# Kernel optimization log

Measured on AMD Instinct MI355X. Metric: run time of the kernel, lower is better.

The kernel has to match this reference:

```python
import jax, jax.numpy as jnp
from jax import lax
import numpy as np


def _gru_cell(x, h, wih, whh, bih, bhh):
    # torch.nn.GRUCell math: gates split order (r, z, n)
    gi = x @ wih.T + bih          # (N, 3H)
    gh = h @ whh.T + bhh          # (N, 3H)
    ir, iz, i_n = jnp.split(gi, 3, axis=-1)
    hr, hz, h_n = jnp.split(gh, 3, axis=-1)
    r = jax.nn.sigmoid(ir + hr)
    z = jax.nn.sigmoid(iz + hz)
    n = jnp.tanh(i_n + r * h_n)
    return (1.0 - z) * n + z * h


def _dilated_gru(x, dilation, wih, whh, bih, bhh):
    # h_i depends on h_{i-dilation} -> `dilation` independent chains,
    # scanned jointly with a carried state of shape (B*dilation, H).
    B, S, I = x.shape
    H = whh.shape[1]
    nc = S // dilation  # assumes S % dilation == 0
    xr = x.reshape(B, nc, dilation, I).transpose(1, 0, 2, 3).reshape(nc, B * dilation, I)

    def step(h, xt):
        hn = _gru_cell(xt, h, wih, whh, bih, bhh)
        return hn, hn

    h0 = jnp.zeros((B * dilation, H), x.dtype)
    _, ys = lax.scan(step, h0, xr)  # (nc, B*dilation, H)
    return ys.reshape(nc, B, dilation, H).transpose(1, 0, 2, 3).reshape(B, S, H)


def _encoder(data, fparams, bparams, dilations):
    outs = []
    x = data
    for p, d in zip(fparams, dilations):
        x = _dilated_gru(x, d, *p)
        outs.append(x[:, -1, :])
    x = data[:, ::-1, :]
    for p, d in zip(bparams, dilations):
        x = _dilated_gru(x, d, *p)
        outs.append(x[:, -1, :])
    return jnp.concatenate(outs, axis=1)  # (B, 2*sum(hidden_sizes)) = (B, 400)


def setup_inputs() -> dict:
    key = jax.random.key(0)
    ks = jax.random.split(key, 7)
    B, S = 1024, 512
    sizes = [(1, 100), (100, 50), (50, 50)]  # (input_size, hidden_size) per layer

    def cell(k, iS, H):
        k1, k2, k3, k4 = jax.random.split(k, 4)
        s = 1.0 / np.sqrt(H)  # torch GRUCell init: U(-1/sqrt(H), 1/sqrt(H))
        u = lambda kk, shp: jax.random.uniform(kk, shp, jnp.float32, -s, s)
        return u(k1, (3 * H, iS)), u(k2, (3 * H, H)), u(k3, (3 * H,)), u(k4, (3 * H,))

    d = {"data": jax.random.normal(ks[0], (B, S, 1), jnp.float32)}
    for i, nm in enumerate(["f1", "f2", "f3", "b1", "b2", "b3"]):
        iS, H = sizes[i % 3]
        w1, w2, bb1, bb2 = cell(ks[i + 1], iS, H)
        d[nm + "_wih"] = w1
        d[nm + "_whh"] = w2
        d[nm + "_bih"] = bb1
        d[nm + "_bhh"] = bb2
    return d


def reference(data,
              f1_wih, f1_whh, f1_bih, f1_bhh,
              f2_wih, f2_whh, f2_bih, f2_bhh,
              f3_wih, f3_whh, f3_bih, f3_bhh,
              b1_wih, b1_whh, b1_bih, b1_bhh,
              b2_wih, b2_whh, b2_bih, b2_bhh,
              b3_wih, b3_whh, b3_bih, b3_bhh):
    dilations = (1, 4, 16)
    fparams = [(f1_wih, f1_whh, f1_bih, f1_bhh),
               (f2_wih, f2_whh, f2_bih, f2_bhh),
               (f3_wih, f3_whh, f3_bih, f3_bhh)]
    bparams = [(b1_wih, b1_whh, b1_bih, b1_bhh),
               (b2_wih, b2_whh, b2_bih, b2_bhh),
               (b3_wih, b3_whh, b3_bih, b3_bhh)]
    return _encoder(data, fparams, bparams, dilations)
```

## Files before the change

### kernel.cpp

```cpp
#include <hip/hip_runtime.h>
#include <math.h>

typedef short  s16x8 __attribute__((ext_vector_type(8)));
typedef float  f32x4 __attribute__((ext_vector_type(4)));

static __device__ __forceinline__ float sigf(float x){ return 1.0f/(1.0f+__expf(-x)); }
static __device__ __forceinline__ float tanhf_fast(float x){
  float ax=fabsf(x); float e=__expf(-2.0f*ax); float t=(1.0f-e)/(1.0f+e); return copysignf(t,x);
}
static __device__ __forceinline__ unsigned short f2bf(float x){
  unsigned int u = __float_as_uint(x);
  unsigned int r = (u + 0x7FFFu + ((u >> 16) & 1u)) >> 16;
  return (unsigned short)r;
}
static __device__ __forceinline__ float bf2f(unsigned short b){
  return __uint_as_float(((unsigned int)b) << 16);
}
static __device__ __forceinline__ unsigned int cvt_pk_bf16(float a, float b){
  unsigned int r;
  asm("v_cvt_pk_bf16_f32 %0, %1, %2" : "=v"(r) : "v"(a), "v"(b));
  return r;
}
static __device__ __forceinline__ void fast_barrier(){
  asm volatile("s_waitcnt lgkmcnt(0)" ::: "memory");
// ... 6 lines not shown
}
static __device__ __forceinline__ float rsum4(float v){
  return v + __int_as_float(__builtin_amdgcn_ds_swizzle(__float_as_int(v), 0x101F));
}
static __device__ __forceinline__ float sel4(int c, float4 v){
  float r=v.x; r=(c==1)?v.y:r; r=(c==2)?v.z:r; r=(c==3)?v.w:r; return r;
}

static __device__ __forceinline__ void load_afrag(const float* __restrict__ whh,
                                                  int gate, int tile, int l, int kc,
                                                  s16x8& hi, s16x8& lo){
  const int r  = tile*16 + (l & 15);
  const int kb = kc*32 + (l >> 4)*8;
  #pragma unroll
  for (int j = 0; j < 8; ++j){
    const int k = kb + j;
    const float wv = (r < 100 && k < 100) ? whh[(size_t)(gate*100 + r)*100 + k] : 0.0f;
    const unsigned short hb = f2bf(wv);
    hi[j] = (short)hb;
    lo[j] = (short)f2bf(wv - bf2f(hb));
  }
}

__global__ __launch_bounds__(448, 2)
void gru_l1(const float* __restrict__ data,
            const float* __restrict__ wih_f, const float* __restrict__ whh_f,
            const float* __restrict__ bih_f, const float* __restrict__ bhh_f,
            const float* __restrict__ wih_b, const float* __restrict__ whh_b,
            const float* __restrict__ bih_b, const float* __restrict__ bhh_b,
            float* __restrict__ x1f, float* __restrict__ x1b,
            float* __restrict__ out)
{
  const int dir   = (int)(blockIdx.x >> 6);
  const int blk16 = (int)(blockIdx.x & 63);
  const int t     = (int)threadIdx.x;
  const float* __restrict__ wih = dir ? wih_b : wih_f;
  const float* __restrict__ whh = dir ? whh_b : whh_f;
  const float* __restrict__ bih = dir ? bih_b : bih_f;
  const float* __restrict__ bhh = dir ? bhh_b : bhh_f;
  float* __restrict__ x1 = dir ? x1b : x1f;
  const int obase = dir ? 200 : 0;
  const int b0 = blk16 * 16;

  __shared__ __align__(16) unsigned short hBhi[2][16][136];
  __shared__ __align__(16) unsigned short hBlo[2][16][136];
  __shared__ __align__(16) float xs[512][16];

  for (int i = t; i < 8192; i += 448){
    const int c  = i >> 9;
    const int sL = i & 511;
    xs[sL][c] = data[(size_t)(b0 + c)*512 + (size_t)(dir ? (511 - sL) : sL)];
  }
  { unsigned short* ph = (unsigned short*)hBhi;
    unsigned short* pl = (unsigned short*)hBlo;
    for (int i = t; i < 2*16*136; i += 448){ ph[i] = 0; pl[i] = 0; } }

  const int l  = t & 63;
  const int W  = t >> 6;

  s16x8 AH00,AH01,AH02,AH03, AH10,AH11,AH12,AH13, AH20,AH21,AH22,AH23;
  s16x8 AL00,AL01,AL02,AL03, AL10,AL11,AL12,AL13, AL20,AL21,AL22,AL23;
  #define LDA(G,KC) load_afrag(whh, G, W, l, KC, AH##G##KC, AL##G##KC);
  LDA(0,0) LDA(0,1) LDA(0,2) LDA(0,3)
  LDA(1,0) LDA(1,1) LDA(1,2) LDA(1,3)
  LDA(2,0) LDA(2,1) LDA(2,2) LDA(2,3)
  #undef LDA

  const int mg  = (l >> 4) * 4;
  const int u0  = W*16 + mg;
  const bool uvalid = (u0 < 100);
  const int u0c = uvalid ? u0 : 96;
  const int c   = l & 15;
  const f32x4 wxr4 = *(const f32x4*)&wih[u0c];
  const f32x4 wxz4 = *(const f32x4*)&wih[100 + u0c];
  const f32x4 wxn4 = *(const f32x4*)&wih[200 + u0c];
  const f32x4 bcr4 = *(const f32x4*)&bih[u0c]       + *(const f32x4*)&bhh[u0c];
  const f32x4 bcz4 = *(const f32x4*)&bih[100 + u0c] + *(const f32x4*)&bhh[100 + u0c];
  const f32x4 bxn4 = *(const f32x4*)&bih[200 + u0c];
  const f32x4 bhn4 = *(const f32x4*)&bhh[200 + u0c];
  f32x4 hprev = {0.f,0.f,0.f,0.f};

  __syncthreads();

  const int bn = c;
  const int bg = (l >> 4)*8;

  #pragma unroll 1
  for (int s = 0; s < 512; ++s){
    const int cur = s & 1, nxt = cur ^ 1;

    const s16x8 BH0 = *(const s16x8*)&hBhi[cur][bn][ 0 + bg];
    const s16x8 BL0 = *(const s16x8*)&hBlo[cur][bn][ 0 + bg];
    const s16x8 BH1 = *(const s16x8*)&hBhi[cur][bn][32 + bg];
    const s16x8 BL1 = *(const s16x8*)&hBlo[cur][bn][32 + bg];
    const s16x8 BH2 = *(const s16x8*)&hBhi[cur][bn][64 + bg];
    const s16x8 BL2 = *(const s16x8*)&hBlo[cur][bn][64 + bg];
    const s16x8 BH3 = *(const s16x8*)&hBhi[cur][bn][96 + bg];
    const s16x8 BL3 = *(const s16x8*)&hBlo[cur][bn][96 + bg];

    f32x4 Ca0={0.f,0.f,0.f,0.f}, Cb0={0.f,0.f,0.f,0.f};
    f32x4 Ca1={0.f,0.f,0.f,0.f}, Cb1={0.f,0.f,0.f,0.f};
    f32x4 Ca2={0.f,0.f,0.f,0.f}, Cb2={0.f,0.f,0.f,0.f};
    #define MM(ACC,G,KC) \
      ACC = __builtin_amdgcn_mfma_f32_16x16x32_bf16(AL##G##KC, BH##KC, ACC, 0, 0, 0); \
      ACC = __builtin_amdgcn_mfma_f32_16x16x32_bf16(AH##G##KC, BL##KC, ACC, 0, 0, 0); \
      ACC = __builtin_amdgcn_mfma_f32_16x16x32_bf16(AH##G##KC, BH##KC, ACC, 0, 0, 0);
    MM(Ca0,0,0) MM(Ca1,1,0) MM(Ca2,2,0)
    MM(Cb0,0,2) MM(Cb1,1,2) MM(Cb2,2,2)
    MM(Ca0,0,1) MM(Ca1,1,1) MM(Ca2,2,1)
    MM(Cb0,0,3) MM(Cb1,1,3) MM(Cb2,2,3)
    #undef MM
    const f32x4 sr = Ca0 + Cb0;
    const f32x4 sz = Ca1 + Cb1;
    const f32x4 sn = Ca2 + Cb2;

    const float xc = xs[s][c];
    f32x4 hn;
    #define FIN(I) { \
      const float rr = sigf(sr[I] + fmaf(wxr4[I], xc, bcr4[I])); \
      const float zz = sigf(sz[I] + fmaf(wxz4[I], xc, bcz4[I])); \
      const float nn = tanhf_fast(fmaf(wxn4[I], xc, bxn4[I]) + rr*(sn[I] + bhn4[I])); \
      hn[I] = nn + zz*(hprev[I] - nn); }
    FIN(0) FIN(1) FIN(2) FIN(3)
    #undef FIN
    hprev = hn;

    if (uvalid){
      const unsigned int px = cvt_pk_bf16(hn[0], hn[1]);
      const unsigned int py = cvt_pk_bf16(hn[2], hn[3]);
      const float l0 = hn[0] - __uint_as_float(px << 16);
      const float l1 = hn[1] - __uint_as_float(px & 0xFFFF0000u);
      const float l2 = hn[2] - __uint_as_float(py << 16);
      const float l3 = hn[3] - __uint_as_float(py & 0xFFFF0000u);
      uint2 vhi; vhi.x = px; vhi.y = py;
      uint2 vlo; vlo.x = cvt_pk_bf16(l0, l1); vlo.y = cvt_pk_bf16(l2, l3);
      *(uint2*)&hBhi[nxt][c][u0] = vhi;
      *(uint2*)&hBlo[nxt][c][u0] = vlo;
      if ((s & 3) == 3){
        const int cs = s >> 2;
        const int ch = b0 + c;
        const size_t base = (((size_t)cs*256 + (ch >> 2))*100);
        x1[(base + u0 + 0)*4 + (ch & 3)] = hn[0];
        x1[(base + u0 + 1)*4 + (ch & 3)] = hn[1];
        x1[(base + u0 + 2)*4 + (ch & 3)] = hn[2];
        x1[(base + u0 + 3)*4 + (ch & 3)] = hn[3];
      }
      if (s == 511){
        const int ch = b0 + c;
        *(f32x4*)&out[(size_t)ch*400 + obase + u0] = hn;
      }
    }
    fast_barrier();
  }
}

static __device__ __forceinline__ float l2w(const float* __restrict__ wih,
                                            const float* __restrict__ whh,
                                            int sec, int r, int k){
  if (r >= 50) return 0.f;
  if (sec == 2) return (k < 100) ? wih[(size_t)(100 + r)*100 + k] : 0.f;
  if (sec == 3) return (k >= 104 && k < 154) ? whh[(size_t)(100 + r)*50 + (k - 104)] : 0.f;
  const int ro = (sec == 1) ? 50 : 0;
  if (k < 100) return wih[(size_t)(ro + r)*100 + k];
  if (k >= 104 && k < 154) return whh[(size_t)(ro + r)*50 + (k - 104)];
  return 0.f;
}
static __device__ __forceinline__ void l2_afrag(const float* __restrict__ wih,
                                                const float* __restrict__ whh,
                                                int sec, int tile, int l, int kc,
                                                s16x8& hi, s16x8& lo){
  const int r  = tile*16 + (l & 15);
  const int kb = kc*32 + (l >> 4)*8;
  #pragma unroll
  for (int j = 0; j < 8; ++j){
    const float wv = l2w(wih, whh, sec, r, kb + j);
    const unsigned short hb = f2bf(wv);
    hi[j] = (short)hb;
    lo[j] = (short)f2bf(wv - bf2f(hb));
  }
}

__global__ __launch_bounds__(256, 1)
void gru_l2(const float* __restrict__ x1f, const float* __restrict__ x1b,
            const float* __restrict__ wih_f, const float* __restrict__ whh_f,
            const float* __restrict__ bih_f, const float* __restrict__ bhh_f,
            const float* __restrict__ wih_b, const float* __restrict__ whh_b,
            const float* __restrict__ bih_b, const float* __restrict__ bhh_b,
            float* __restrict__ x2f, float* __restrict__ x2b,
            float* __restrict__ out)
{
  const int dir   = (int)(blockIdx.x >> 6);
  const int blk16 = (int)(blockIdx.x & 63);
  const int t     = (int)threadIdx.x;
  const float* __restrict__ wih = dir ? wih_b : wih_f;
  const float* __restrict__ whh = dir ? whh_b : whh_f;
  const float* __restrict__ bih = dir ? bih_b : bih_f;
  const float* __restrict__ bhh = dir ? bhh_b : bhh_f;
  const float* __restrict__ x1 = dir ? x1b : x1f;
  float* __restrict__ x2 = dir ? x2b : x2f;
  const int obase = dir ? 300 : 100;
  const int b0 = blk16 * 16;

  __shared__ __align__(16) unsigned short hBhi[2][16][168];
  __shared__ __align__(16) unsigned short hBlo[2][16][168];

  { unsigned short* ph = (unsigned short*)hBhi;
    unsigned short* pl = (unsigned short*)hBlo;
    for (int i = t; i < 2*16*168; i += 256){ ph[i] = 0; pl[i] = 0; } }

  const int l = t & 63;
  const int W = t >> 6;

  s16x8 AH00,AH01,AH02,AH03,AH04, AH10,AH11,AH12,AH13,AH14,
        AH20,AH21,AH22,AH23,AH24, AH30,AH31,AH32,AH33,AH34;
  s16x8 AL00,AL01,AL02,AL03,AL04, AL10,AL11,AL12,AL13,AL14,
        AL20,AL21,AL22,AL23,AL24, AL30,AL31,AL32,AL33,AL34;
  #define LDA(SE,KC) l2_afrag(wih, whh, SE, W, l, KC, AH##SE##KC, AL##SE##KC);
  LDA(0,0) LDA(0,1) LDA(0,2) LDA(0,3) LDA(0,4)
  LDA(1,0) LDA(1,1) LDA(1,2) LDA(1,3) LDA(1,4)
  LDA(2,0) LDA(2,1) LDA(2,2) LDA(2,3) LDA(2,4)
  LDA(3,0) LDA(3,1) LDA(3,2) LDA(3,3) LDA(3,4)
  #undef LDA

  const int mg = (l >> 4) * 4;
  const int c  = l & 15;
  const int u0 = W*16 + mg;
  const int ch = b0 + c;
  f32x4 bcr, bcz, bxn, bhn;
  #pragma unroll
  for (int i = 0; i < 4; ++i){
    const int u = (u0 + i < 50) ? (u0 + i) : 49;
    bcr[i] = bih[u]      + bhh[u];
    bcz[i] = bih[50 + u] + bhh[50 + u];
    bxn[i] = bih[100 + u];
    bhn[i] = bhh[100 + u];
  }
  const bool vH = (u0 < 50);
  f32x4 hp = {0.f,0.f,0.f,0.f};

  float* px = x2 + (((size_t)(ch >> 2))*50 + u0)*4 + (ch & 3);
  const size_t X2STRIDE = (size_t)256*50*4;

  const int oct  = t >> 4;
  const int cc   = t & 15;
  const bool stg = (t < 208);
  const int u0x  = oct * 8;

  __syncthreads();

  if (stg){
    const float* p = x1 + ((size_t)0*256 + (b0 >> 2) + (cc >> 2))*400 + (cc & 3);
    float xv[8];
    #pragma unroll
    for (int j = 0; j < 8; ++j){
      const int uu = u0x + j;
      xv[j] = (uu < 100) ? p[4*uu] : 0.f;
    }
    unsigned int h0 = cvt_pk_bf16(xv[0], xv[1]);
    unsigned int h1 = cvt_pk_bf16(xv[2], xv[3]);
    unsigned int h2 = cvt_pk_bf16(xv[4], xv[5]);
    unsigned int h3 = cvt_pk_bf16(xv[6], xv[7]);
    uint4 vhi; vhi.x=h0; vhi.y=h1; vhi.z=h2; vhi.w=h3;
    uint4 vlo;
    vlo.x = cvt_pk_bf16(xv[0]-__uint_as_float(h0<<16), xv[1]-__uint_as_float(h0&0xFFFF0000u));
    vlo.y = cvt_pk_bf16(xv[2]-__uint_as_float(h1<<16), xv[3]-__uint_as_float(h1&0xFFFF0000u));
    vlo.z = cvt_pk_bf16(xv[4]-__uint_as_float(h2<<16), xv[5]-__uint_as_float(h2&0xFFFF0000u));
    vlo.w = cvt_pk_bf16(xv[6]-__uint_as_float(h3<<16), xv[7]-__uint_as_float(h3&0xFFFF0000u));
    *(uint4*)&hBhi[0][cc][u0x] = vhi;
    *(uint4*)&hBlo[0][cc][u0x] = vlo;
  }
  __syncthreads();

  const int bn = c;
  const int bg = (l >> 4)*8;

  #pragma unroll 1
  for (int s = 0; s < 128; ++s){
    const int cur = s & 1, nxt = cur ^ 1;

    float xv0=0,xv1=0,xv2=0,xv3=0,xv4=0,xv5=0,xv6=0,xv7=0;
    if (stg){
      const int st = (s + 1 < 128) ? (s + 1) : 127;
      const float* p = x1 + ((size_t)st*256 + (b0 >> 2) + (cc >> 2))*400 + (cc & 3);
      #define XL(J, V) { const int uu = u0x + (J); \
        V = (uu < 100) ? p[4*uu] : 0.f; }
      XL(0,xv0) XL(1,xv1) XL(2,xv2) XL(3,xv3) XL(4,xv4) XL(5,xv5) XL(6,xv6) XL(7,xv7)
      #undef XL
    }

    const s16x8 BH0 = *(const s16x8*)&hBhi[cur][bn][  0 + bg];
    const s16x8 BL0 = *(const s16x8*)&hBlo[cur][bn][  0 + bg];
    const s16x8 BH1 = *(const s16x8*)&hBhi[cur][bn][ 32 + bg];
    const s16x8 BL1 = *(const s16x8*)&hBlo[cur][bn][ 32 + bg];
    const s16x8 BH2 = *(const s16x8*)&hBhi[cur][bn][ 64 + bg];
    const s16x8 BL2 = *(const s16x8*)&hBlo[cur][bn][ 64 + bg];
    const s16x8 BH3 = *(const s16x8*)&hBhi[cur][bn][ 96 + bg];
    const s16x8 BL3 = *(const s16x8*)&hBlo[cur][bn][ 96 + bg];
    const s16x8 BH4 = *(const s16x8*)&hBhi[cur][bn][128 + bg];
    const s16x8 BL4 = *(const s16x8*)&hBlo[cur][bn][128 + bg];

    f32x4 CrA={0.f,0.f,0.f,0.f}, CzA={0.f,0.f,0.f,0.f}, CxA={0.f,0.f,0.f,0.f}, ChA={0.f,0.f,0.f,0.f};
    f32x4 CrB={0.f,0.f,0.f,0.f}, CzB={0.f,0.f,0.f,0.f}, CxB={0.f,0.f,0.f,0.f}, ChB={0.f,0.f,0.f,0.f};
    #define MF(ACC,A,B) ACC = __builtin_amdgcn_mfma_f32_16x16x32_bf16(A, B, ACC, 0, 0, 0);
    #define G4(SET,KC,AOP,BOP) \
      MF(Cr##SET, AOP##0##KC, BOP##KC) MF(Cz##SET, AOP##1##KC, BOP##KC) \
      MF(Cx##SET, AOP##2##KC, BOP##KC) MF(Ch##SET, AOP##3##KC, BOP##KC)
    G4(A,0,AL,BH) G4(B,3,AL,BH) G4(A,1,AL,BH) G4(B,4,AL,BH) G4(A,2,AL,BH)
    G4(A,0,AH,BL) G4(B,3,AH,BL) G4(A,1,AH,BL) G4(B,4,AH,BL) G4(A,2,AH,BL)
    G4(A,0,AH,BH) G4(B,3,AH,BH) G4(A,1,AH,BH) G4(B,4,AH,BH) G4(A,2,AH,BH)
    #undef G4
    #undef MF
    const f32x4 Cr = CrA + CrB;
    const f32x4 Cz = CzA + CzB;
    const f32x4 Cx = CxA + CxB;
    const f32x4 Ch = ChA + ChB;

    f32x4 hn;
    #define FIN(I) { \
      const float rr = sigf(Cr[I] + bcr[I]); \
      const float zz = sigf(Cz[I] + bcz[I]); \
      const float nn = tanhf_fast(Cx[I] + bxn[I] + rr*(Ch[I] + bhn[I])); \
      hn[I] = nn + zz*(hp[I] - nn); }
    FIN(0) FIN(1) FIN(2) FIN(3)
    #undef FIN
    hp = hn;

    if (vH){
      const unsigned int p0 = cvt_pk_bf16(hn[0], hn[1]);
      const unsigned int p1 = cvt_pk_bf16(hn[2], hn[3]);
      const float l0 = hn[0] - __uint_as_float(p0 << 16);
      const float l1 = hn[1] - __uint_as_float(p0 & 0xFFFF0000u);
      const float l2 = hn[2] - __uint_as_float(p1 << 16);
      const float l3 = hn[3] - __uint_as_float(p1 & 0xFFFF0000u);
      uint2 whi; whi.x = p0; whi.y = p1;
      uint2 wlo; wlo.x = cvt_pk_bf16(l0, l1); wlo.y = cvt_pk_bf16(l2, l3);
      *(uint2*)&hBhi[nxt][c][104 + u0] = whi;
      *(uint2*)&hBlo[nxt][c][104 + u0] = wlo;
      if ((s & 3) == 3){
        if (u0 + 0 < 50) px[ 0] = hn[0];
        if (u0 + 1 < 50) px[ 4] = hn[1];
        if (u0 + 2 < 50) px[ 8] = hn[2];
        if (u0 + 3 < 50) px[12] = hn[3];
        px += X2STRIDE;
      }
      if (s == 127){
        if (u0 + 0 < 50) out[(size_t)ch*400 + obase + u0 + 0] = hn[0];
        if (u0 + 1 < 50) out[(size_t)ch*400 + obase + u0 + 1] = hn[1];
        if (u0 + 2 < 50) out[(size_t)ch*400 + obase + u0 + 2] = hn[2];
        if (u0 + 3 < 50) out[(size_t)ch*400 + obase + u0 + 3] = hn[3];
      }
    }

    if (stg){
      unsigned int h0 = cvt_pk_bf16(xv0, xv1);
      unsigned int h1 = cvt_pk_bf16(xv2, xv3);
      unsigned int h2 = cvt_pk_bf16(xv4, xv5);
      unsigned int h3 = cvt_pk_bf16(xv6, xv7);
      uint4 vhi; vhi.x=h0; vhi.y=h1; vhi.z=h2; vhi.w=h3;
      uint4 vlo;
      vlo.x = cvt_pk_bf16(xv0-__uint_as_float(h0<<16), xv1-__uint_as_float(h0&0xFFFF0000u));
      vlo.y = cvt_pk_bf16(xv2-__uint_as_float(h1<<16), xv3-__uint_as_float(h1&0xFFFF0000u));
      vlo.z = cvt_pk_bf16(xv4-__uint_as_float(h2<<16), xv5-__uint_as_float(h2&0xFFFF0000u));
      vlo.w = cvt_pk_bf16(xv6-__uint_as_float(h3<<16), xv7-__uint_as_float(h3&0xFFFF0000u));
      *(uint4*)&hBhi[nxt][cc][u0x] = vhi;
      *(uint4*)&hBlo[nxt][cc][u0x] = vlo;
    }
    fast_barrier();
  }
}

__global__ __launch_bounds__(512, 4)
void gru_l3(const float* __restrict__ x2f, const float* __restrict__ x2b,
            const float* __restrict__ wih_f, const float* __restrict__ whh_f,
            const float* __restrict__ bih_f, const float* __restrict__ bhh_f,
            const float* __restrict__ wih_b, const float* __restrict__ whh_b,
            const float* __restrict__ bih_b, const float* __restrict__ bhh_b,
            float* __restrict__ out)
{
  const int dir = (int)(blockIdx.x >> 8);
  const int blk = (int)(blockIdx.x & 255);
  const int t   = (int)threadIdx.x;
  const float* __restrict__ wih = dir ? wih_b : wih_f;
  const float* __restrict__ whh = dir ? whh_b : whh_f;
  const float* __restrict__ bih = dir ? bih_b : bih_f;
  const float* __restrict__ bhh = dir ? bhh_b : bhh_f;
  const float* __restrict__ x2 = dir ? x2b : x2f;
  const int obase = dir ? 350 : 150;
  const int b0 = blk * 4;

  __shared__ __align__(16) float xh[2][104][4];
// ... 85 lines not shown
  const float* f2_whh = (const float*)d_in[6];
  const float* f2_bih = (const float*)d_in[7];
  const float* f2_bhh = (const float*)d_in[8];
  const float* f3_wih = (const float*)d_in[9];
  const float* f3_whh = (const float*)d_in[10];
  const float* f3_bih = (const float*)d_in[11];
  const float* f3_bhh = (const float*)d_in[12];
  const float* b1_wih = (const float*)d_in[13];
  const float* b1_whh = (const float*)d_in[14];
  const float* b1_bih = (const float*)d_in[15];
  const float* b1_bhh = (const float*)d_in[16];
  const float* b2_wih = (const float*)d_in[17];
  const float* b2_whh = (const float*)d_in[18];
  const float* b2_bih = (const float*)d_in[19];
  const float* b2_bhh = (const float*)d_in[20];
  const float* b3_wih = (const float*)d_in[21];
  const float* b3_whh = (const float*)d_in[22];
  const float* b3_bih = (const float*)d_in[23];
  const float* b3_bhh = (const float*)d_in[24];
  float* out = (float*)d_out;

  const size_t X1N = (size_t)128 * 256 * 100 * 4;
  const size_t X2N = (size_t)32 * 256 * 50 * 4;
  if (ws_size < (2 * X1N + 2 * X2N) * sizeof(float)) return;
  float* wsf = (float*)d_ws;
  float* x1f = wsf;
  float* x1b = wsf + X1N;
  float* x2f = wsf + 2 * X1N;
  float* x2b = wsf + 2 * X1N + X2N;

  gru_l1<<<dim3(128), dim3(448), 0, stream>>>(
      data, f1_wih, f1_whh, f1_bih, f1_bhh,
      b1_wih, b1_whh, b1_bih, b1_bhh, x1f, x1b, out);
  gru_l2<<<dim3(128), dim3(256), 0, stream>>>(
      x1f, x1b, f2_wih, f2_whh, f2_bih, f2_bhh,
      b2_wih, b2_whh, b2_bih, b2_bhh, x2f, x2b, out);
  gru_l3<<<dim3(512), dim3(512), 0, stream>>>(
      x2f, x2b, f3_wih, f3_whh, f3_bih, f3_bhh,
      b3_wih, b3_whh, b3_bih, b3_bhh, out);
}
```

Measured before the change: 1.024 ms.

## Fuse layer-1 and layer-2 GRU kernels with flag-based producer-consumer pipelining

Merges the layer-1 and layer-2 kernels into one launch of 256 blocks. The first 128 blocks run layer 1 and publish per-block progress flags with release stores every 4 steps. The other 128 blocks run layer 2 and spin on those flags with acquire loads before reading each x1 chunk. This lets layer 2 overlap with layer 1 instead of waiting for it to finish, removing most of the layer-2 serial time. The cost is extra barriers and a vmcnt wait in layer 1, spin-wait overhead, and reliance on all 256 blocks being co-resident to avoid deadlock, with a spin budget as a fallback.

```diff
diff --git a/kernel.cpp b/kernel.cpp
--- a/kernel.cpp
+++ b/kernel.cpp
@@ -52,138 +52,6 @@
   }
 }
 
-__global__ __launch_bounds__(448, 2)
-void gru_l1(const float* __restrict__ data,
-            const float* __restrict__ wih_f, const float* __restrict__ whh_f,
-            const float* __restrict__ bih_f, const float* __restrict__ bhh_f,
-            const float* __restrict__ wih_b, const float* __restrict__ whh_b,
-            const float* __restrict__ bih_b, const float* __restrict__ bhh_b,
-            float* __restrict__ x1f, float* __restrict__ x1b,
-            float* __restrict__ out)
-{
-  const int dir   = (int)(blockIdx.x >> 6);
-  const int blk16 = (int)(blockIdx.x & 63);
-  const int t     = (int)threadIdx.x;
-  const float* __restrict__ wih = dir ? wih_b : wih_f;
-  const float* __restrict__ whh = dir ? whh_b : whh_f;
-  const float* __restrict__ bih = dir ? bih_b : bih_f;
-  const float* __restrict__ bhh = dir ? bhh_b : bhh_f;
-  float* __restrict__ x1 = dir ? x1b : x1f;
-  const int obase = dir ? 200 : 0;
-  const int b0 = blk16 * 16;
-
-  __shared__ __align__(16) unsigned short hBhi[2][16][136];
-  __shared__ __align__(16) unsigned short hBlo[2][16][136];
-  __shared__ __align__(16) float xs[512][16];
-
-  for (int i = t; i < 8192; i += 448){
-    const int c  = i >> 9;
-    const int sL = i & 511;
-    xs[sL][c] = data[(size_t)(b0 + c)*512 + (size_t)(dir ? (511 - sL) : sL)];
-  }
-  { unsigned short* ph = (unsigned short*)hBhi;
-    unsigned short* pl = (unsigned short*)hBlo;
-    for (int i = t; i < 2*16*136; i += 448){ ph[i] = 0; pl[i] = 0; } }
-
-  const int l  = t & 63;
-  const int W  = t >> 6;
-
-  s16x8 AH00,AH01,AH02,AH03, AH10,AH11,AH12,AH13, AH20,AH21,AH22,AH23;
-  s16x8 AL00,AL01,AL02,AL03, AL10,AL11,AL12,AL13, AL20,AL21,AL22,AL23;
-  #define LDA(G,KC) load_afrag(whh, G, W, l, KC, AH##G##KC, AL##G##KC);
-  LDA(0,0) LDA(0,1) LDA(0,2) LDA(0,3)
-  LDA(1,0) LDA(1,1) LDA(1,2) LDA(1,3)
-  LDA(2,0) LDA(2,1) LDA(2,2) LDA(2,3)
-  #undef LDA
-
-  const int mg  = (l >> 4) * 4;
-  const int u0  = W*16 + mg;
-  const bool uvalid = (u0 < 100);
-  const int u0c = uvalid ? u0 : 96;
-  const int c   = l & 15;
-  const f32x4 wxr4 = *(const f32x4*)&wih[u0c];
-  const f32x4 wxz4 = *(const f32x4*)&wih[100 + u0c];
-  const f32x4 wxn4 = *(const f32x4*)&wih[200 + u0c];
-  const f32x4 bcr4 = *(const f32x4*)&bih[u0c]       + *(const f32x4*)&bhh[u0c];
-  const f32x4 bcz4 = *(const f32x4*)&bih[100 + u0c] + *(const f32x4*)&bhh[100 + u0c];
-  const f32x4 bxn4 = *(const f32x4*)&bih[200 + u0c];
-  const f32x4 bhn4 = *(const f32x4*)&bhh[200 + u0c];
-  f32x4 hprev = {0.f,0.f,0.f,0.f};
-
-  __syncthreads();
-
-  const int bn = c;
-  const int bg = (l >> 4)*8;
-
-  #pragma unroll 1
-  for (int s = 0; s < 512; ++s){
-    const int cur = s & 1, nxt = cur ^ 1;
-
-    const s16x8 BH0 = *(const s16x8*)&hBhi[cur][bn][ 0 + bg];
-    const s16x8 BL0 = *(const s16x8*)&hBlo[cur][bn][ 0 + bg];
-    const s16x8 BH1 = *(const s16x8*)&hBhi[cur][bn][32 + bg];
-    const s16x8 BL1 = *(const s16x8*)&hBlo[cur][bn][32 + bg];
-    const s16x8 BH2 = *(const s16x8*)&hBhi[cur][bn][64 + bg];
-    const s16x8 BL2 = *(const s16x8*)&hBlo[cur][bn][64 + bg];
-    const s16x8 BH3 = *(const s16x8*)&hBhi[cur][bn][96 + bg];
-    const s16x8 BL3 = *(const s16x8*)&hBlo[cur][bn][96 + bg];
-
-    f32x4 Ca0={0.f,0.f,0.f,0.f}, Cb0={0.f,0.f,0.f,0.f};
-    f32x4 Ca1={0.f,0.f,0.f,0.f}, Cb1={0.f,0.f,0.f,0.f};
-    f32x4 Ca2={0.f,0.f,0.f,0.f}, Cb2={0.f,0.f,0.f,0.f};
-    #define MM(ACC,G,KC) \
-      ACC = __builtin_amdgcn_mfma_f32_16x16x32_bf16(AL##G##KC, BH##KC, ACC, 0, 0, 0); \
-      ACC = __builtin_amdgcn_mfma_f32_16x16x32_bf16(AH##G##KC, BL##KC, ACC, 0, 0, 0); \
-      ACC = __builtin_amdgcn_mfma_f32_16x16x32_bf16(AH##G##KC, BH##KC, ACC, 0, 0, 0);
-    MM(Ca0,0,0) MM(Ca1,1,0) MM(Ca2,2,0)
-    MM(Cb0,0,2) MM(Cb1,1,2) MM(Cb2,2,2)
-    MM(Ca0,0,1) MM(Ca1,1,1) MM(Ca2,2,1)
-    MM(Cb0,0,3) MM(Cb1,1,3) MM(Cb2,2,3)
-    #undef MM
-    const f32x4 sr = Ca0 + Cb0;
-    const f32x4 sz = Ca1 + Cb1;
-    const f32x4 sn = Ca2 + Cb2;
-
-    const float xc = xs[s][c];
-    f32x4 hn;
-    #define FIN(I) { \
-      const float rr = sigf(sr[I] + fmaf(wxr4[I], xc, bcr4[I])); \
-      const float zz = sigf(sz[I] + fmaf(wxz4[I], xc, bcz4[I])); \
-      const float nn = tanhf_fast(fmaf(wxn4[I], xc, bxn4[I]) + rr*(sn[I] + bhn4[I])); \
-      hn[I] = nn + zz*(hprev[I] - nn); }
-    FIN(0) FIN(1) FIN(2) FIN(3)
-    #undef FIN
-    hprev = hn;
-
-    if (uvalid){
-      const unsigned int px = cvt_pk_bf16(hn[0], hn[1]);
-      const unsigned int py = cvt_pk_bf16(hn[2], hn[3]);
-      const float l0 = hn[0] - __uint_as_float(px << 16);
-      const float l1 = hn[1] - __uint_as_float(px & 0xFFFF0000u);
-      const float l2 = hn[2] - __uint_as_float(py << 16);
-      const float l3 = hn[3] - __uint_as_float(py & 0xFFFF0000u);
-      uint2 vhi; vhi.x = px; vhi.y = py;
-      uint2 vlo; vlo.x = cvt_pk_bf16(l0, l1); vlo.y = cvt_pk_bf16(l2, l3);
-      *(uint2*)&hBhi[nxt][c][u0] = vhi;
-      *(uint2*)&hBlo[nxt][c][u0] = vlo;
-      if ((s & 3) == 3){
-        const int cs = s >> 2;
-        const int ch = b0 + c;
-        const size_t base = (((size_t)cs*256 + (ch >> 2))*100);
-        x1[(base + u0 + 0)*4 + (ch & 3)] = hn[0];
-        x1[(base + u0 + 1)*4 + (ch & 3)] = hn[1];
-        x1[(base + u0 + 2)*4 + (ch & 3)] = hn[2];
-        x1[(base + u0 + 3)*4 + (ch & 3)] = hn[3];
-      }
-      if (s == 511){
-        const int ch = b0 + c;
-        *(f32x4*)&out[(size_t)ch*400 + obase + u0] = hn;
-      }
-    }
-    fast_barrier();
-  }
-}
-
 static __device__ __forceinline__ float l2w(const float* __restrict__ wih,
                                             const float* __restrict__ whh,
                                             int sec, int r, int k){
@@ -210,192 +78,346 @@
   }
 }
 
-__global__ __launch_bounds__(256, 1)
-void gru_l2(const float* __restrict__ x1f, const float* __restrict__ x1b,
-            const float* __restrict__ wih_f, const float* __restrict__ whh_f,
-            const float* __restrict__ bih_f, const float* __restrict__ bhh_f,
-            const float* __restrict__ wih_b, const float* __restrict__ whh_b,
-            const float* __restrict__ bih_b, const float* __restrict__ bhh_b,
-            float* __restrict__ x2f, float* __restrict__ x2b,
-            float* __restrict__ out)
+__global__ __launch_bounds__(448, 2)
+void gru_fused(const float* __restrict__ data,
+               const float* __restrict__ w1ih_f, const float* __restrict__ w1hh_f,
+               const float* __restrict__ b1ih_f, const float* __restrict__ b1hh_f,
+               const float* __restrict__ w1ih_b, const float* __restrict__ w1hh_b,
+               const float* __restrict__ b1ih_b, const float* __restrict__ b1hh_b,
+               const float* __restrict__ w2ih_f, const float* __restrict__ w2hh_f,
+               const float* __restrict__ b2ih_f, const float* __restrict__ b2hh_f,
+               const float* __restrict__ w2ih_b, const float* __restrict__ w2hh_b,
+               const float* __restrict__ b2ih_b, const float* __restrict__ b2hh_b,
+               float* __restrict__ x1f, float* __restrict__ x1b,
+               float* __restrict__ x2f, float* __restrict__ x2b,
+               int* __restrict__ flags,
+               float* __restrict__ out)
 {
-  const int dir   = (int)(blockIdx.x >> 6);
-  const int blk16 = (int)(blockIdx.x & 63);
-  const int t     = (int)threadIdx.x;
-  const float* __restrict__ wih = dir ? wih_b : wih_f;
-  const float* __restrict__ whh = dir ? whh_b : whh_f;
-  const float* __restrict__ bih = dir ? bih_b : bih_f;
-  const float* __restrict__ bhh = dir ? bhh_b : bhh_f;
-  const float* __restrict__ x1 = dir ? x1b : x1f;
-  float* __restrict__ x2 = dir ? x2b : x2f;
-  const int obase = dir ? 300 : 100;
-  const int b0 = blk16 * 16;
-
-  __shared__ __align__(16) unsigned short hBhi[2][16][168];
-  __shared__ __align__(16) unsigned short hBlo[2][16][168];
-
-  { unsigned short* ph = (unsigned short*)hBhi;
-    unsigned short* pl = (unsigned short*)hBlo;
-    for (int i = t; i < 2*16*168; i += 256){ ph[i] = 0; pl[i] = 0; } }
-
-  const int l = t & 63;
-  const int W = t >> 6;
-
-  s16x8 AH00,AH01,AH02,AH03,AH04, AH10,AH11,AH12,AH13,AH14,
-        AH20,AH21,AH22,AH23,AH24, AH30,AH31,AH32,AH33,AH34;
-  s16x8 AL00,AL01,AL02,AL03,AL04, AL10,AL11,AL12,AL13,AL14,
-        AL20,AL21,AL22,AL23,AL24, AL30,AL31,AL32,AL33,AL34;
-  #define LDA(SE,KC) l2_afrag(wih, whh, SE, W, l, KC, AH##SE##KC, AL##SE##KC);
-  LDA(0,0) LDA(0,1) LDA(0,2) LDA(0,3) LDA(0,4)
-  LDA(1,0) LDA(1,1) LDA(1,2) LDA(1,3) LDA(1,4)
-  LDA(2,0) LDA(2,1) LDA(2,2) LDA(2,3) LDA(2,4)
-  LDA(3,0) LDA(3,1) LDA(3,2) LDA(3,3) LDA(3,4)
-  #undef LDA
-
-  const int mg = (l >> 4) * 4;
-  const int c  = l & 15;
-  const int u0 = W*16 + mg;
-  const int ch = b0 + c;
-  f32x4 bcr, bcz, bxn, bhn;
-  #pragma unroll
-  for (int i = 0; i < 4; ++i){
-    const int u = (u0 + i < 50) ? (u0 + i) : 49;
-    bcr[i] = bih[u]      + bhh[u];
-    bcz[i] = bih[50 + u] + bhh[50 + u];
-    bxn[i] = bih[100 + u];
-    bhn[i] = bhh[100 + u];
-  }
-  const bool vH = (u0 < 50);
-  f32x4 hp = {0.f,0.f,0.f,0.f};
-
-  float* px = x2 + (((size_t)(ch >> 2))*50 + u0)*4 + (ch & 3);
-  const size_t X2STRIDE = (size_t)256*50*4;
-
-  const int oct  = t >> 4;
-  const int cc   = t & 15;
-  const bool stg = (t < 208);
-  const int u0x  = oct * 8;
-
-  __syncthreads();
-
-  if (stg){
-    const float* p = x1 + ((size_t)0*256 + (b0 >> 2) + (cc >> 2))*400 + (cc & 3);
-    float xv[8];
+  __shared__ __align__(16) char smem[50176];
+  const int t = (int)threadIdx.x;
+
+  if (blockIdx.x < 128){
+    const int dir   = (int)(blockIdx.x >> 6);
+    const int blk16 = (int)(blockIdx.x & 63);
+    const int fid   = (int)blockIdx.x;
+    const float* __restrict__ wih = dir ? w1ih_b : w1ih_f;
+    const float* __restrict__ whh = dir ? w1hh_b : w1hh_f;
+    const float* __restrict__ bih = dir ? b1ih_b : b1ih_f;
+    const float* __restrict__ bhh = dir ? b1hh_b : b1hh_f;
+    float* __restrict__ x1 = dir ? x1b : x1f;
+    const int obase = dir ? 200 : 0;
+    const int b0 = blk16 * 16;
+
+    unsigned short (*hBhi)[16][136] = (unsigned short (*)[16][136])(smem);
+    unsigned short (*hBlo)[16][136] = (unsigned short (*)[16][136])(smem + 8704);
+    float (*xs)[16]                 = (float (*)[16])(smem + 17408);
+
+    for (int i = t; i < 8192; i += 448){
+      const int c  = i >> 9;
+      const int sL = i & 511;
+      xs[sL][c] = data[(size_t)(b0 + c)*512 + (size_t)(dir ? (511 - sL) : sL)];
+    }
+    { unsigned short* ph = (unsigned short*)smem;
+      for (int i = t; i < 2*2*16*136; i += 448) ph[i] = 0; }
+
+    const int l  = t & 63;
+    const int W  = t >> 6;
+
+    s16x8 AH00,AH01,AH02,AH03, AH10,AH11,AH12,AH13, AH20,AH21,AH22,AH23;
+    s16x8 AL00,AL01,AL02,AL03, AL10,AL11,AL12,AL13, AL20,AL21,AL22,AL23;
+    #define LDA(G,KC) load_afrag(whh, G, W, l, KC, AH##G##KC, AL##G##KC);
+    LDA(0,0) LDA(0,1) LDA(0,2) LDA(0,3)
+    LDA(1,0) LDA(1,1) LDA(1,2) LDA(1,3)
+    LDA(2,0) LDA(2,1) LDA(2,2) LDA(2,3)
+    #undef LDA
+
+    const int mg  = (l >> 4) * 4;
+    const int u0  = W*16 + mg;
+    const bool uvalid = (u0 < 100);
+    const int u0c = uvalid ? u0 : 96;
+    const int c   = l & 15;
+    const f32x4 wxr4 = *(const f32x4*)&wih[u0c];
+    const f32x4 wxz4 = *(const f32x4*)&wih[100 + u0c];
+    const f32x4 wxn4 = *(const f32x4*)&wih[200 + u0c];
+    const f32x4 bcr4 = *(const f32x4*)&bih[u0c]       + *(const f32x4*)&bhh[u0c];
+    const f32x4 bcz4 = *(const f32x4*)&bih[100 + u0c] + *(const f32x4*)&bhh[100 + u0c];
+    const f32x4 bxn4 = *(const f32x4*)&bih[200 + u0c];
+    const f32x4 bhn4 = *(const f32x4*)&bhh[200 + u0c];
+    f32x4 hprev = {0.f,0.f,0.f,0.f};
+
+    __syncthreads();
+
+    const int bn = c;
+    const int bg = (l >> 4)*8;
+
+    #pragma unroll 1
+    for (int s = 0; s < 512; ++s){
+      const int cur = s & 1, nxt = cur ^ 1;
+
+      const s16x8 BH0 = *(const s16x8*)&hBhi[cur][bn][ 0 + bg];
+      const s16x8 BL0 = *(const s16x8*)&hBlo[cur][bn][ 0 + bg];
+      const s16x8 BH1 = *(const s16x8*)&hBhi[cur][bn][32 + bg];
+      const s16x8 BL1 = *(const s16x8*)&hBlo[cur][bn][32 + bg];
+      const s16x8 BH2 = *(const s16x8*)&hBhi[cur][bn][64 + bg];
+      const s16x8 BL2 = *(const s16x8*)&hBlo[cur][bn][64 + bg];
+      const s16x8 BH3 = *(const s16x8*)&hBhi[cur][bn][96 + bg];
+      const s16x8 BL3 = *(const s16x8*)&hBlo[cur][bn][96 + bg];
+
+      f32x4 Ca0={0.f,0.f,0.f,0.f}, Cb0={0.f,0.f,0.f,0.f};
+      f32x4 Ca1={0.f,0.f,0.f,0.f}, Cb1={0.f,0.f,0.f,0.f};
+      f32x4 Ca2={0.f,0.f,0.f,0.f}, Cb2={0.f,0.f,0.f,0.f};
+      #define MM(ACC,G,KC) \
+        ACC = __builtin_amdgcn_mfma_f32_16x16x32_bf16(AL##G##KC, BH##KC, ACC, 0, 0, 0); \
+        ACC = __builtin_amdgcn_mfma_f32_16x16x32_bf16(AH##G##KC, BL##KC, ACC, 0, 0, 0); \
+        ACC = __builtin_amdgcn_mfma_f32_16x16x32_bf16(AH##G##KC, BH##KC, ACC, 0, 0, 0);
+      MM(Ca0,0,0) MM(Ca1,1,0) MM(Ca2,2,0)
+      MM(Cb0,0,2) MM(Cb1,1,2) MM(Cb2,2,2)
+      MM(Ca0,0,1) MM(Ca1,1,1) MM(Ca2,2,1)
+      MM(Cb0,0,3) MM(Cb1,1,3) MM(Cb2,2,3)
+      #undef MM
+      const f32x4 sr = Ca0 + Cb0;
+      const f32x4 sz = Ca1 + Cb1;
+      const f32x4 sn = Ca2 + Cb2;
+
+      const float xc = xs[s][c];
+      f32x4 hn;
+      #define FIN(I) { \
+        const float rr = sigf(sr[I] + fmaf(wxr4[I], xc, bcr4[I])); \
+        const float zz = sigf(sz[I] + fmaf(wxz4[I], xc, bcz4[I])); \
+        const float nn = tanhf_fast(fmaf(wxn4[I], xc, bxn4[I]) + rr*(sn[I] + bhn4[I])); \
+        hn[I] = nn + zz*(hprev[I] - nn); }
+      FIN(0) FIN(1) FIN(2) FIN(3)
+      #undef FIN
+      hprev = hn;
+
+      if (uvalid){
+        const unsigned int px = cvt_pk_bf16(hn[0], hn[1]);
+        const unsigned int py = cvt_pk_bf16(hn[2], hn[3]);
+        const float l0 = hn[0] - __uint_as_float(px << 16);
+        const float l1 = hn[1] - __uint_as_float(px & 0xFFFF0000u);
+        const float l2 = hn[2] - __uint_as_float(py << 16);
+        const float l3 = hn[3] - __uint_as_float(py & 0xFFFF0000u);
+        uint2 vhi; vhi.x = px; vhi.y = py;
+        uint2 vlo; vlo.x = cvt_pk_bf16(l0, l1); vlo.y = cvt_pk_bf16(l2, l3);
+        *(uint2*)&hBhi[nxt][c][u0] = vhi;
+        *(uint2*)&hBlo[nxt][c][u0] = vlo;
+        if ((s & 3) == 3){
+          const int cs = s >> 2;
+          const int ch = b0 + c;
+          const size_t base = (((size_t)cs*256 + (ch >> 2))*100);
+          x1[(base + u0 + 0)*4 + (ch & 3)] = hn[0];
+          x1[(base + u0 + 1)*4 + (ch & 3)] = hn[1];
+          x1[(base + u0 + 2)*4 + (ch & 3)] = hn[2];
+          x1[(base + u0 + 3)*4 + (ch & 3)] = hn[3];
+        }
+        if (s == 511){
+          const int ch = b0 + c;
+          *(f32x4*)&out[(size_t)ch*400 + obase + u0] = hn;
+        }
+      }
+      if ((s & 3) == 3){
+        asm volatile("s_waitcnt vmcnt(0)" ::: "memory");
+        __builtin_amdgcn_s_barrier();
+        if (t == 0){
+          __hip_atomic_store(&flags[fid], (s >> 2) + 1,
+                             __ATOMIC_RELEASE, __HIP_MEMORY_SCOPE_AGENT);
+        }
+      }
+      fast_barrier();
+    }
+  } else {
+    const int kb    = (int)blockIdx.x - 128;
+    const int dir   = kb >> 6;
+    const int blk16 = kb & 63;
+    const int fid   = kb;
+    const float* __restrict__ wih = dir ? w2ih_b : w2ih_f;
+    const float* __restrict__ whh = dir ? w2hh_b : w2hh_f;
+    const float* __restrict__ bih = dir ? b2ih_b : b2ih_f;
+    const float* __restrict__ bhh = dir ? b2hh_b : b2hh_f;
+    const float* __restrict__ x1 = dir ? x1b : x1f;
+    float* __restrict__ x2 = dir ? x2b : x2f;
+    const int obase = dir ? 300 : 100;
+    const int b0 = blk16 * 16;
+
+    unsigned short (*hBhi)[16][168] = (unsigned short (*)[16][168])(smem);
+    unsigned short (*hBlo)[16][168] = (unsigned short (*)[16][168])(smem + 10752);
+
+    { unsigned short* ph = (unsigned short*)smem;
+      for (int i = t; i < 2*2*16*168; i += 448) ph[i] = 0; }
+
+    const int l = t & 63;
+    const int W = t >> 6;
+
+    s16x8 AH00,AH01,AH02,AH03,AH04, AH10,AH11,AH12,AH13,AH14,
+          AH20,AH21,AH22,AH23,AH24, AH30,AH31,AH32,AH33,AH34;
+    s16x8 AL00,AL01,AL02,AL03,AL04, AL10,AL11,AL12,AL13,AL14,
+          AL20,AL21,AL22,AL23,AL24, AL30,AL31,AL32,AL33,AL34;
+    #define LDA(SE,KC) l2_afrag(wih, whh, SE, W, l, KC, AH##SE##KC, AL##SE##KC);
+    LDA(0,0) LDA(0,1) LDA(0,2) LDA(0,3) LDA(0,4)
+    LDA(1,0) LDA(1,1) LDA(1,2) LDA(1,3) LDA(1,4)
+    LDA(2,0) LDA(2,1) LDA(2,2) LDA(2,3) LDA(2,4)
+    LDA(3,0) LDA(3,1) LDA(3,2) LDA(3,3) LDA(3,4)
+    #undef LDA
+
+    const int mg = (l >> 4) * 4;
+    const int c  = l & 15;
+    const int u0 = W*16 + mg;
+    const int ch = b0 + c;
+    f32x4 bcr, bcz, bxn, bhn;
     #pragma unroll
-    for (int j = 0; j < 8; ++j){
-      const int uu = u0x + j;
-      xv[j] = (uu < 100) ? p[4*uu] : 0.f;
-    }
-    unsigned int h0 = cvt_pk_bf16(xv[0], xv[1]);
-    unsigned int h1 = cvt_pk_bf16(xv[2], xv[3]);
-    unsigned int h2 = cvt_pk_bf16(xv[4], xv[5]);
-    unsigned int h3 = cvt_pk_bf16(xv[6], xv[7]);
-    uint4 vhi; vhi.x=h0; vhi.y=h1; vhi.z=h2; vhi.w=h3;
-    uint4 vlo;
-    vlo.x = cvt_pk_bf16(xv[0]-__uint_as_float(h0<<16), xv[1]-__uint_as_float(h0&0xFFFF0000u));
-    vlo.y = cvt_pk_bf16(xv[2]-__uint_as_float(h1<<16), xv[3]-__uint_as_float(h1&0xFFFF0000u));
-    vlo.z = cvt_pk_bf16(xv[4]-__uint_as_float(h2<<16), xv[5]-__uint_as_float(h2&0xFFFF0000u));
-    vlo.w = cvt_pk_bf16(xv[6]-__uint_as_float(h3<<16), xv[7]-__uint_as_float(h3&0xFFFF0000u));
-    *(uint4*)&hBhi[0][cc][u0x] = vhi;
-    *(uint4*)&hBlo[0][cc][u0x] = vlo;
-  }
-  __syncthreads();
-
-  const int bn = c;
-  const int bg = (l >> 4)*8;
-
-  #pragma unroll 1
-  for (int s = 0; s < 128; ++s){
-    const int cur = s & 1, nxt = cur ^ 1;
-
-    float xv0=0,xv1=0,xv2=0,xv3=0,xv4=0,xv5=0,xv6=0,xv7=0;
+    for (int i = 0; i < 4; ++i){
+      const int u = (u0 + i < 50) ? (u0 + i) : 49;
+      bcr[i] = bih[u]      + bhh[u];
+      bcz[i] = bih[50 + u] + bhh[50 + u];
+      bxn[i] = bih[100 + u];
+      bhn[i] = bhh[100 + u];
+    }
+    const bool vH = (u0 < 50);
+    f32x4 hp = {0.f,0.f,0.f,0.f};
+
+    float* px = x2 + (((size_t)(ch >> 2))*50 + u0)*4 + (ch & 3);
+    const size_t X2STRIDE = (size_t)256*50*4;
+
+    const int oct  = t >> 4;
+    const int cc   = t & 15;
+    const bool stg = (t < 208);
+    const int u0x  = oct * 8;
+
+    int spin_budget = 1 << 22;
+
+    __syncthreads();
+
+    if (t == 0){
+      while (__hip_atomic_load(&flags[fid], __ATOMIC_ACQUIRE, __HIP_MEMORY_SCOPE_AGENT) < 1
+             && spin_budget > 0){ __builtin_amdgcn_s_sleep(8); --spin_budget; }
+    }
+    fast_barrier();
     if (stg){
-      const int st = (s + 1 < 128) ? (s + 1) : 127;
-      const float* p = x1 + ((size_t)st*256 + (b0 >> 2) + (cc >> 2))*400 + (cc & 3);
-      #define XL(J, V) { const int uu = u0x + (J); \
-        V = (uu < 100) ? p[4*uu] : 0.f; }
-      XL(0,xv0) XL(1,xv1) XL(2,xv2) XL(3,xv3) XL(4,xv4) XL(5,xv5) XL(6,xv6) XL(7,xv7)
-      #undef XL
-    }
-
-    const s16x8 BH0 = *(const s16x8*)&hBhi[cur][bn][  0 + bg];
-    const s16x8 BL0 = *(const s16x8*)&hBlo[cur][bn][  0 + bg];
-    const s16x8 BH1 = *(const s16x8*)&hBhi[cur][bn][ 32 + bg];
-    const s16x8 BL1 = *(const s16x8*)&hBlo[cur][bn][ 32 + bg];
-    const s16x8 BH2 = *(const s16x8*)&hBhi[cur][bn][ 64 + bg];
-    const s16x8 BL2 = *(const s16x8*)&hBlo[cur][bn][ 64 + bg];
-    const s16x8 BH3 = *(const s16x8*)&hBhi[cur][bn][ 96 + bg];
-    const s16x8 BL3 = *(const s16x8*)&hBlo[cur][bn][ 96 + bg];
-    const s16x8 BH4 = *(const s16x8*)&hBhi[cur][bn][128 + bg];
-    const s16x8 BL4 = *(const s16x8*)&hBlo[cur][bn][128 + bg];
-
-    f32x4 CrA={0.f,0.f,0.f,0.f}, CzA={0.f,0.f,0.f,0.f}, CxA={0.f,0.f,0.f,0.f}, ChA={0.f,0.f,0.f,0.f};
-    f32x4 CrB={0.f,0.f,0.f,0.f}, CzB={0.f,0.f,0.f,0.f}, CxB={0.f,0.f,0.f,0.f}, ChB={0.f,0.f,0.f,0.f};
-    #define MF(ACC,A,B) ACC = __builtin_amdgcn_mfma_f32_16x16x32_bf16(A, B, ACC, 0, 0, 0);
-    #define G4(SET,KC,AOP,BOP) \
-      MF(Cr##SET, AOP##0##KC, BOP##KC) MF(Cz##SET, AOP##1##KC, BOP##KC) \
-      MF(Cx##SET, AOP##2##KC, BOP##KC) MF(Ch##SET, AOP##3##KC, BOP##KC)
-    G4(A,0,AL,BH) G4(B,3,AL,BH) G4(A,1,AL,BH) G4(B,4,AL,BH) G4(A,2,AL,BH)
-    G4(A,0,AH,BL) G4(B,3,AH,BL) G4(A,1,AH,BL) G4(B,4,AH,BL) G4(A,2,AH,BL)
-    G4(A,0,AH,BH) G4(B,3,AH,BH) G4(A,1,AH,BH) G4(B,4,AH,BH) G4(A,2,AH,BH)
-    #undef G4
-    #undef MF
-    const f32x4 Cr = CrA + CrB;
-    const f32x4 Cz = CzA + CzB;
-    const f32x4 Cx = CxA + CxB;
-    const f32x4 Ch = ChA + ChB;
-
-    f32x4 hn;
-    #define FIN(I) { \
-      const float rr = sigf(Cr[I] + bcr[I]); \
-      const float zz = sigf(Cz[I] + bcz[I]); \
-      const float nn = tanhf_fast(Cx[I] + bxn[I] + rr*(Ch[I] + bhn[I])); \
-      hn[I] = nn + zz*(hp[I] - nn); }
-    FIN(0) FIN(1) FIN(2) FIN(3)
-    #undef FIN
-    hp = hn;
-
-    if (vH){
-      const unsigned int p0 = cvt_pk_bf16(hn[0], hn[1]);
-      const unsigned int p1 = cvt_pk_bf16(hn[2], hn[3]);
-      const float l0 = hn[0] - __uint_as_float(p0 << 16);
-      const float l1 = hn[1] - __uint_as_float(p0 & 0xFFFF0000u);
-      const float l2 = hn[2] - __uint_as_float(p1 << 16);
-      const float l3 = hn[3] - __uint_as_float(p1 & 0xFFFF0000u);
-      uint2 whi; whi.x = p0; whi.y = p1;
-      uint2 wlo; wlo.x = cvt_pk_bf16(l0, l1); wlo.y = cvt_pk_bf16(l2, l3);
-      *(uint2*)&hBhi[nxt][c][104 + u0] = whi;
-      *(uint2*)&hBlo[nxt][c][104 + u0] = wlo;
-      if ((s & 3) == 3){
-        if (u0 + 0 < 50) px[ 0] = hn[0];
-        if (u0 + 1 < 50) px[ 4] = hn[1];
-        if (u0 + 2 < 50) px[ 8] = hn[2];
-        if (u0 + 3 < 50) px[12] = hn[3];
-        px += X2STRIDE;
-      }
-      if (s == 127){
-        if (u0 + 0 < 50) out[(size_t)ch*400 + obase + u0 + 0] = hn[0];
-        if (u0 + 1 < 50) out[(size_t)ch*400 + obase + u0 + 1] = hn[1];
-        if (u0 + 2 < 50) out[(size_t)ch*400 + obase + u0 + 2] = hn[2];
-        if (u0 + 3 < 50) out[(size_t)ch*400 + obase + u0 + 3] = hn[3];
-      }
-    }
-
-    if (stg){
-      unsigned int h0 = cvt_pk_bf16(xv0, xv1);
-      unsigned int h1 = cvt_pk_bf16(xv2, xv3);
-      unsigned int h2 = cvt_pk_bf16(xv4, xv5);
-      unsigned int h3 = cvt_pk_bf16(xv6, xv7);
+      const float* p = x1 + ((size_t)0*256 + (b0 >> 2) + (cc >> 2))*400 + (cc & 3);
+      float xv[8];
+      #pragma unroll
+      for (int j = 0; j < 8; ++j){
+        const int uu = u0x + j;
+        xv[j] = (uu < 100) ? p[4*uu] : 0.f;
+      }
+      unsigned int h0 = cvt_pk_bf16(xv[0], xv[1]);
+      unsigned int h1 = cvt_pk_bf16(xv[2], xv[3]);
+      unsigned int h2 = cvt_pk_bf16(xv[4], xv[5]);
+      unsigned int h3 = cvt_pk_bf16(xv[6], xv[7]);
       uint4 vhi; vhi.x=h0; vhi.y=h1; vhi.z=h2; vhi.w=h3;
       uint4 vlo;
-      vlo.x = cvt_pk_bf16(xv0-__uint_as_float(h0<<16), xv1-__uint_as_float(h0&0xFFFF0000u));
-      vlo.y = cvt_pk_bf16(xv2-__uint_as_float(h1<<16), xv3-__uint_as_float(h1&0xFFFF0000u));
-      vlo.z = cvt_pk_bf16(xv4-__uint_as_float(h2<<16), xv5-__uint_as_float(h2&0xFFFF0000u));
-      vlo.w = cvt_pk_bf16(xv6-__uint_as_float(h3<<16), xv7-__uint_as_float(h3&0xFFFF0000u));
-      *(uint4*)&hBhi[nxt][cc][u0x] = vhi;
-      *(uint4*)&hBlo[nxt][cc][u0x] = vlo;
-    }
-    fast_barrier();
+      vlo.x = cvt_pk_bf16(xv[0]-__uint_as_float(h0<<16), xv[1]-__uint_as_float(h0&0xFFFF0000u));
+      vlo.y = cvt_pk_bf16(xv[2]-__uint_as_float(h1<<16), xv[3]-__uint_as_float(h1&0xFFFF0000u));
+      vlo.z = cvt_pk_bf16(xv[4]-__uint_as_float(h2<<16), xv[5]-__uint_as_float(h2&0xFFFF0000u));
+      vlo.w = cvt_pk_bf16(xv[6]-__uint_as_float(h3<<16), xv[7]-__uint_as_float(h3&0xFFFF0000u));
+      *(uint4*)&hBhi[0][cc][u0x] = vhi;
+      *(uint4*)&hBlo[0][cc][u0x] = vlo;
+    }
+    __syncthreads();
+
+    const int bn = c;
+    const int bg = (l >> 4)*8;
+
+    #pragma unroll 1
+    for (int s = 0; s < 128; ++s){
+      const int cur = s & 1, nxt = cur ^ 1;
+
+      { const int want = (s + 2 < 128) ? (s + 2) : 128;
+        if (t == 0){
+          while (__hip_atomic_load(&flags[fid], __ATOMIC_ACQUIRE, __HIP_MEMORY_SCOPE_AGENT) < want
+                 && spin_budget > 0){ __builtin_amdgcn_s_sleep(8); --spin_budget; }
+        }
+        fast_barrier(); }
+
+      float xv0=0,xv1=0,xv2=0,xv3=0,xv4=0,xv5=0,xv6=0,xv7=0;
+      if (stg){
+        const int st = (s + 1 < 128) ? (s + 1) : 127;
+        const float* p = x1 + ((size_t)st*256 + (b0 >> 2) + (cc >> 2))*400 + (cc & 3);
+        #define XL(J, V) { const int uu = u0x + (J); \
+          V = (uu < 100) ? p[4*uu] : 0.f; }
+        XL(0,xv0) XL(1,xv1) XL(2,xv2) XL(3,xv3) XL(4,xv4) XL(5,xv5) XL(6,xv6) XL(7,xv7)
+        #undef XL
+      }
+
+      const s16x8 BH0 = *(const s16x8*)&hBhi[cur][bn][  0 + bg];
+      const s16x8 BL0 = *(const s16x8*)&hBlo[cur][bn][  0 + bg];
+      const s16x8 BH1 = *(const s16x8*)&hBhi[cur][bn][ 32 + bg];
+      const s16x8 BL1 = *(const s16x8*)&hBlo[cur][bn][ 32 + bg];
+      const s16x8 BH2 = *(const s16x8*)&hBhi[cur][bn][ 64 + bg];
+      const s16x8 BL2 = *(const s16x8*)&hBlo[cur][bn][ 64 + bg];
+      const s16x8 BH3 = *(const s16x8*)&hBhi[cur][bn][ 96 + bg];
+      const s16x8 BL3 = *(const s16x8*)&hBlo[cur][bn][ 96 + bg];
+      const s16x8 BH4 = *(const s16x8*)&hBhi[cur][bn][128 + bg];
+      const s16x8 BL4 = *(const s16x8*)&hBlo[cur][bn][128 + bg];
+
+      f32x4 CrA={0.f,0.f,0.f,0.f}, CzA={0.f,0.f,0.f,0.f}, CxA={0.f,0.f,0.f,0.f}, ChA={0.f,0.f,0.f,0.f};
+      f32x4 CrB={0.f,0.f,0.f,0.f}, CzB={0.f,0.f,0.f,0.f}, CxB={0.f,0.f,0.f,0.f}, ChB={0.f,0.f,0.f,0.f};
+      #define MF(ACC,A,B) ACC = __builtin_amdgcn_mfma_f32_16x16x32_bf16(A, B, ACC, 0, 0, 0);
+      #define G4(SET,KC,AOP,BOP) \
+        MF(Cr##SET, AOP##0##KC, BOP##KC) MF(Cz##SET, AOP##1##KC, BOP##KC) \
+        MF(Cx##SET, AOP##2##KC, BOP##KC) MF(Ch##SET, AOP##3##KC, BOP##KC)
+      G4(A,0,AL,BH) G4(B,3,AL,BH) G4(A,1,AL,BH) G4(B,4,AL,BH) G4(A,2,AL,BH)
+      G4(A,0,AH,BL) G4(B,3,AH,BL) G4(A,1,AH,BL) G4(B,4,AH,BL) G4(A,2,AH,BL)
+      G4(A,0,AH,BH) G4(B,3,AH,BH) G4(A,1,AH,BH) G4(B,4,AH,BH) G4(A,2,AH,BH)
+      #undef G4
+      #undef MF
+      const f32x4 Cr = CrA + CrB;
+      const f32x4 Cz = CzA + CzB;
+      const f32x4 Cx = CxA + CxB;
+      const f32x4 Ch = ChA + ChB;
+
+      f32x4 hn;
+      #define FIN(I) { \
+        const float rr = sigf(Cr[I] + bcr[I]); \
+        const float zz = sigf(Cz[I] + bcz[I]); \
+        const float nn = tanhf_fast(Cx[I] + bxn[I] + rr*(Ch[I] + bhn[I])); \
+        hn[I] = nn + zz*(hp[I] - nn); }
+      FIN(0) FIN(1) FIN(2) FIN(3)
+      #undef FIN
+      hp = hn;
+
+      if (vH){
+        const unsigned int p0 = cvt_pk_bf16(hn[0], hn[1]);
+        const unsigned int p1 = cvt_pk_bf16(hn[2], hn[3]);
+        const float l0 = hn[0] - __uint_as_float(p0 << 16);
+        const float l1 = hn[1] - __uint_as_float(p0 & 0xFFFF0000u);
+        const float l2 = hn[2] - __uint_as_float(p1 << 16);
+        const float l3 = hn[3] - __uint_as_float(p1 & 0xFFFF0000u);
+        uint2 whi; whi.x = p0; whi.y = p1;
+        uint2 wlo; wlo.x = cvt_pk_bf16(l0, l1); wlo.y = cvt_pk_bf16(l2, l3);
+        *(uint2*)&hBhi[nxt][c][104 + u0] = whi;
+        *(uint2*)&hBlo[nxt][c][104 + u0] = wlo;
+        if ((s & 3) == 3){
+          if (u0 + 0 < 50) px[ 0] = hn[0];
+          if (u0 + 1 < 50) px[ 4] = hn[1];
+          if (u0 + 2 < 50) px[ 8] = hn[2];
+          if (u0 + 3 < 50) px[12] = hn[3];
+          px += X2STRIDE;
+        }
+        if (s == 127){
+          if (u0 + 0 < 50) out[(size_t)ch*400 + obase + u0 + 0] = hn[0];
+          if (u0 + 1 < 50) out[(size_t)ch*400 + obase + u0 + 1] = hn[1];
+          if (u0 + 2 < 50) out[(size_t)ch*400 + obase + u0 + 2] = hn[2];
+          if (u0 + 3 < 50) out[(size_t)ch*400 + obase + u0 + 3] = hn[3];
+        }
+      }
+
+      if (stg){
+        unsigned int h0 = cvt_pk_bf16(xv0, xv1);
+        unsigned int h1 = cvt_pk_bf16(xv2, xv3);
+        unsigned int h2 = cvt_pk_bf16(xv4, xv5);
+        unsigned int h3 = cvt_pk_bf16(xv6, xv7);
+        uint4 vhi; vhi.x=h0; vhi.y=h1; vhi.z=h2; vhi.w=h3;
+        uint4 vlo;
+        vlo.x = cvt_pk_bf16(xv0-__uint_as_float(h0<<16), xv1-__uint_as_float(h0&0xFFFF0000u));
+        vlo.y = cvt_pk_bf16(xv2-__uint_as_float(h1<<16), xv3-__uint_as_float(h1&0xFFFF0000u));
+        vlo.z = cvt_pk_bf16(xv4-__uint_as_float(h2<<16), xv5-__uint_as_float(h2&0xFFFF0000u));
+        vlo.w = cvt_pk_bf16(xv6-__uint_as_float(h3<<16), xv7-__uint_as_float(h3&0xFFFF0000u));
+        *(uint4*)&hBhi[nxt][cc][u0x] = vhi;
+        *(uint4*)&hBlo[nxt][cc][u0x] = vlo;
+      }
+      fast_barrier();
+    }
   }
 }
 
@@ -527,19 +549,22 @@
 
   const size_t X1N = (size_t)128 * 256 * 100 * 4;
   const size_t X2N = (size_t)32 * 256 * 50 * 4;
-  if (ws_size < (2 * X1N + 2 * X2N) * sizeof(float)) return;
+  const size_t FLN = 128;
+  if (ws_size < (2 * X1N + 2 * X2N) * sizeof(float) + FLN * sizeof(int)) return;
   float* wsf = (float*)d_ws;
   float* x1f = wsf;
   float* x1b = wsf + X1N;
   float* x2f = wsf + 2 * X1N;
   float* x2b = wsf + 2 * X1N + X2N;
-
-  gru_l1<<<dim3(128), dim3(448), 0, stream>>>(
-      data, f1_wih, f1_whh, f1_bih, f1_bhh,
-      b1_wih, b1_whh, b1_bih, b1_bhh, x1f, x1b, out);
-  gru_l2<<<dim3(128), dim3(256), 0, stream>>>(
-      x1f, x1b, f2_wih, f2_whh, f2_bih, f2_bhh,
-      b2_wih, b2_whh, b2_bih, b2_bhh, x2f, x2b, out);
+  int*   flags = (int*)(wsf + 2 * X1N + 2 * X2N);
+
+  hipMemsetAsync(flags, 0, FLN * sizeof(int), stream);
+
+  gru_fused<<<dim3(256), dim3(448), 0, stream>>>(
+      data,
+      f1_wih, f1_whh, f1_bih, f1_bhh, b1_wih, b1_whh, b1_bih, b1_bhh,
+      f2_wih, f2_whh, f2_bih, f2_bhh, b2_wih, b2_whh, b2_bih, b2_bhh,
+      x1f, x1b, x2f, x2b, flags, out);
   gru_l3<<<dim3(512), dim3(512), 0, stream>>>(
       x2f, x2b, f3_wih, f3_whh, f3_bih, f3_bhh,
       b3_wih, b3_whh, b3_bih, b3_bhh, out);
```

Measured after the change: 1.305 ms. 1.28x slower.
